# Optimization experiments

Hardware: AMD Instinct MI355X
Metric: run time of the kernel (lower is better)

The kernel has to match this reference:

```python
import jax, jax.numpy as jnp
import numpy as np

P1 = np.uint32(2654435761)
P2 = np.uint32(805459861)

LEVELS = 16
N_MIN = 16
GROWTH = 1.5
TABLE_SIZE = 524288
FEAT_DIM = 2


def _make_seeds_u32(levels):
    cA = np.uint64(15485907386658061715)
    cB = np.uint64(11400714819323198485)
    ls = np.arange(levels, dtype=np.uint64)
    u = (cA ^ (ls * cB))  # uint64 wraparound
    return (u & np.uint64(0xFFFFFFFF)).astype(np.uint32)


def setup_inputs() -> dict:
    key = jax.random.key(0)
    k1, k2, k3 = jax.random.split(key, 3)
    B = 8
    H = 256
    tile = 1024
    x0 = jax.random.uniform(k1, (B,), dtype=jnp.float32) * (tile - H)
    y0 = jax.random.uniform(k2, (B,), dtype=jnp.float32) * (tile - H)
    tables = jax.random.uniform(k3, (TABLE_SIZE, FEAT_DIM), dtype=jnp.float32,
                                minval=-0.01, maxval=0.01)
    seeds = jnp.asarray(_make_seeds_u32(LEVELS))
    level_N = jnp.asarray(
        [int(round(N_MIN * GROWTH ** l)) for l in range(LEVELS)], dtype=jnp.float32)
    return {"x0": x0, "y0": y0, "tables": tables, "seeds": seeds,
            "level_N": level_N, "memorized_crop_size": H,
            "complete_tile_size": tile}


def _hash2d(ix, iy, seed_u, T):
    # Instant-NGP style spatial hash, uint32 wraparound, per-level seed.
    h = (ix.astype(jnp.uint32) * P1) ^ (iy.astype(jnp.uint32) * P2) ^ seed_u
    return (h % jnp.uint32(T)).astype(jnp.int32)


def reference(x0, y0, tables, seeds, level_N, memorized_crop_size, complete_tile_size):
    B = x0.shape[0]
    H = W = int(memorized_crop_size)
    L = seeds.shape[0]
    T, F = tables.shape
    N = H * W

    xs = jnp.arange(H, dtype=jnp.float32)
    yy, xx = jnp.meshgrid(xs, xs, indexing='ij')          # [H, W]
    pxf = (xx[None] + x0[:, None, None]).reshape(B, N)     # [B, N]
    pyf = (yy[None] + y0[:, None, None]).reshape(B, N)

    scales = level_N / jnp.float32(complete_tile_size)     # [L]
    xyn_x = pxf[:, None, :] * scales[None, :, None]        # [B, L, N]
    xyn_y = pyf[:, None, :] * scales[None, :, None]

    ix0 = jnp.floor(xyn_x).astype(jnp.int32)
    iy0 = jnp.floor(xyn_y).astype(jnp.int32)
    ix1 = ix0 + 1
    iy1 = iy0 + 1
    fx = (xyn_x - ix0)[..., None]                          # [B, L, N, 1]
    fy = (xyn_y - iy0)[..., None]

    s = seeds[None, :, None]                               # [1, L, 1] uint32
    f00 = tables[_hash2d(ix0, iy0, s, T)]                  # [B, L, N, F]
    f10 = tables[_hash2d(ix1, iy0, s, T)]
    f01 = tables[_hash2d(ix0, iy1, s, T)]
    f11 = tables[_hash2d(ix1, iy1, s, T)]

    enc = ((1.0 - fx) * (1.0 - fy) * f00 + fx * (1.0 - fy) * f10
           + (1.0 - fx) * fy * f01 + fx * fy * f11)        # [B, L, N, F]

    enc = jnp.transpose(enc, (0, 2, 1, 3)).reshape(B, H, W, L * F)
    return jnp.transpose(enc, (0, 3, 1, 2))                # [B, L*F, H, W]
```

## Files before the change

kernel.cpp:

```cpp
#include <hip/hip_runtime.h>
#include <stdint.h>

#define HASH_T 524288u
#define HASH_MASK (HASH_T - 1u)
#define PRIME1 2654435761u
#define PRIME2 805459861u

__global__ __launch_bounds__(256) void lia_hashgrid_kernel(
    const float* __restrict__ x0,
    const float* __restrict__ y0,
    const float* __restrict__ tables,
    const uint32_t* __restrict__ seeds,
    const float* __restrict__ level_N,
    const int* __restrict__ tile_p,
    float* __restrict__ out)
{
    const int gid = blockIdx.x * 256 + threadIdx.x;
    const int j = gid & 255;
    const int i = (gid >> 8) & 255;
    const int bh = gid >> 16;
    const int half = bh & 1;
    const int b = bh >> 1;

    const float inv_tile = 1.0f / (float)(*tile_p);
    const float px = (float)j + x0[b];
    const float py = (float)i + y0[b];

    const float2* __restrict__ tab2 = (const float2*)tables;
    float* outp = out + ((size_t)b * 32u + (size_t)half * 16u) * 65536u
                      + (size_t)(i * 256 + j);

    const int lbase = half * 8;

    #pragma unroll
    for (int ll = 0; ll < 8; ++ll) {
        const int l = lbase + ll;
        const float scale = level_N[l] * inv_tile;
        const uint32_t seed = seeds[l];

        const float xn = px * scale;
        const float yn = py * scale;
        const float flx = floorf(xn);
        const float fly = floorf(yn);
        const float fx = xn - flx;
        const float fy = yn - fly;
        const uint32_t ix0 = (uint32_t)(int)flx;
        const uint32_t iy0 = (uint32_t)(int)fly;

        const uint32_t hx0 = ix0 * PRIME1;
        const uint32_t hx1 = hx0 + PRIME1;
        const uint32_t hy0 = iy0 * PRIME2;
        const uint32_t hy1 = hy0 + PRIME2;

        const uint32_t h00 = (hx0 ^ hy0 ^ seed) & HASH_MASK;
        const uint32_t h10 = (hx1 ^ hy0 ^ seed) & HASH_MASK;
        const uint32_t h01 = (hx0 ^ hy1 ^ seed) & HASH_MASK;
        const uint32_t h11 = (hx1 ^ hy1 ^ seed) & HASH_MASK;

        const float2 f00 = tab2[h00];
        const float2 f10 = tab2[h10];
        const float2 f01 = tab2[h01];
        const float2 f11 = tab2[h11];

        const float gx = 1.0f - fx;
        const float gy = 1.0f - fy;
        const float w00 = gx * gy;
        const float w10 = fx * gy;
        const float w01 = gx * fy;
        const float w11 = fx * fy;

        const float e0 = w00 * f00.x + w10 * f10.x + w01 * f01.x + w11 * f11.x;
        const float e1 = w00 * f00.y + w10 * f10.y + w01 * f01.y + w11 * f11.y;

        __builtin_nontemporal_store(e0, &outp[(size_t)(2 * ll) * 65536u]);
        __builtin_nontemporal_store(e1, &outp[(size_t)(2 * ll + 1) * 65536u]);
    }
}

extern "C" void kernel_launch(void* const* d_in, const int* in_sizes, int n_in,
                              void* d_out, int out_size, void* d_ws, size_t ws_size,
                              hipStream_t stream) {
    const float*    x0      = (const float*)d_in[0];
    const float*    y0      = (const float*)d_in[1];
    const float*    tables  = (const float*)d_in[2];
    const uint32_t* seeds   = (const uint32_t*)d_in[3];
    const float*    level_N = (const float*)d_in[4];
    const int*      tile_p  = (const int*)d_in[6];
    float*          out     = (float*)d_out;

    const int B = in_sizes[0];
    const int n_threads = B * 2 * 256 * 256;
    const int n_blocks = n_threads / 256;

    lia_hashgrid_kernel<<<n_blocks, 256, 0, stream>>>(
        x0, y0, tables, seeds, level_N, tile_p, out);
}
```

Before: 70.99 us.

## Process four pixels per thread, sharing corner gathers and vectorizing stores

Each thread now computes four adjacent pixels in x, so coarse levels can gather a small shared set of corner table entries and select among them instead of doing four gathers per pixel. Output stores become 16-byte vector nontemporal stores. Work is split unevenly across the two halves: one half handles levels 0-10 and the other levels 11-15, to balance gather counts. Correctness depends on the assumption that at most one (or four) cell boundaries are crossed within four pixels at those level scales. The grid also shrinks by four, which cuts thread count and occupancy.

```diff
diff --git a/kernel.cpp b/kernel.cpp
--- a/kernel.cpp
+++ b/kernel.cpp
@@ -5,6 +5,8 @@
 #define HASH_MASK (HASH_T - 1u)
 #define PRIME1 2654435761u
 #define PRIME2 805459861u
+
+typedef float f32x4 __attribute__((ext_vector_type(4)));
 
 __global__ __launch_bounds__(256) void lia_hashgrid_kernel(
     const float* __restrict__ x0,
@@ -16,64 +18,161 @@
     float* __restrict__ out)
 {
     const int gid = blockIdx.x * 256 + threadIdx.x;
-    const int j = gid & 255;
-    const int i = (gid >> 8) & 255;
-    const int bh = gid >> 16;
+    const int j0 = (gid & 63) << 2;
+    const int i  = (gid >> 6) & 255;
+    const int bh = gid >> 14;
     const int half = bh & 1;
     const int b = bh >> 1;
 
     const float inv_tile = 1.0f / (float)(*tile_p);
-    const float px = (float)j + x0[b];
+    const float xb = x0[b];
     const float py = (float)i + y0[b];
 
     const float2* __restrict__ tab2 = (const float2*)tables;
-    float* outp = out + ((size_t)b * 32u + (size_t)half * 16u) * 65536u
-                      + (size_t)(i * 256 + j);
+    float* outp = out + (size_t)b * 32u * 65536u + (size_t)(i * 256 + j0);
 
-    const int lbase = half * 8;
+    if (half == 0) {
+        #pragma unroll
+        for (int l = 0; l < 8; ++l) {
+            const float s = level_N[l] * inv_tile;
+            const uint32_t seed = seeds[l];
 
-    #pragma unroll
-    for (int ll = 0; ll < 8; ++ll) {
-        const int l = lbase + ll;
-        const float scale = level_N[l] * inv_tile;
-        const uint32_t seed = seeds[l];
+            const float yn = py * s;
+            const float fy = yn - floorf(yn);
+            const uint32_t iy0 = (uint32_t)(int)floorf(yn);
+            const uint32_t hy0 = iy0 * PRIME2;
+            const uint32_t hy1 = hy0 + PRIME2;
 
-        const float xn = px * scale;
-        const float yn = py * scale;
-        const float flx = floorf(xn);
-        const float fly = floorf(yn);
-        const float fx = xn - flx;
-        const float fy = yn - fly;
-        const uint32_t ix0 = (uint32_t)(int)flx;
-        const uint32_t iy0 = (uint32_t)(int)fly;
+            const float xn0 = ((float)j0 + xb) * s;
+            const float flx0 = floorf(xn0);
+            const uint32_t X = (uint32_t)(int)flx0;
+            const uint32_t hx0 = X * PRIME1;
+            const uint32_t hx1 = hx0 + PRIME1;
+            const uint32_t hx2 = hx1 + PRIME1;
 
-        const uint32_t hx0 = ix0 * PRIME1;
-        const uint32_t hx1 = hx0 + PRIME1;
-        const uint32_t hy0 = iy0 * PRIME2;
-        const uint32_t hy1 = hy0 + PRIME2;
+            const float2 t00 = tab2[(hx0 ^ hy0 ^ seed) & HASH_MASK];
+            const float2 t10 = tab2[(hx1 ^ hy0 ^ seed) & HASH_MASK];
+            const float2 t20 = tab2[(hx2 ^ hy0 ^ seed) & HASH_MASK];
+            const float2 t01 = tab2[(hx0 ^ hy1 ^ seed) & HASH_MASK];
+            const float2 t11 = tab2[(hx1 ^ hy1 ^ seed) & HASH_MASK];
+            const float2 t21 = tab2[(hx2 ^ hy1 ^ seed) & HASH_MASK];
 
-        const uint32_t h00 = (hx0 ^ hy0 ^ seed) & HASH_MASK;
-        const uint32_t h10 = (hx1 ^ hy0 ^ seed) & HASH_MASK;
-        const uint32_t h01 = (hx0 ^ hy1 ^ seed) & HASH_MASK;
-        const uint32_t h11 = (hx1 ^ hy1 ^ seed) & HASH_MASK;
+            const float gy = 1.0f - fy;
+            float e0s[4], e1s[4];
+            #pragma unroll
+            for (int p = 0; p < 4; ++p) {
+                const float xn = ((float)(j0 + p) + xb) * s;
+                const float flx = floorf(xn);
+                const float fx = xn - flx;
+                const bool dd = ((int)flx - (int)flx0) != 0;
+                const float2 f00 = dd ? t10 : t00;
+                const float2 f10 = dd ? t20 : t10;
+                const float2 f01 = dd ? t11 : t01;
+                const float2 f11 = dd ? t21 : t11;
+                const float gx = 1.0f - fx;
+                const float w00 = gx * gy, w10 = fx * gy;
+                const float w01 = gx * fy, w11 = fx * fy;
+                e0s[p] = w00 * f00.x + w10 * f10.x + w01 * f01.x + w11 * f11.x;
+                e1s[p] = w00 * f00.y + w10 * f10.y + w01 * f01.y + w11 * f11.y;
+            }
+            f32x4 v0 = {e0s[0], e0s[1], e0s[2], e0s[3]};
+            f32x4 v1 = {e1s[0], e1s[1], e1s[2], e1s[3]};
+            __builtin_nontemporal_store(v0, (f32x4*)(outp + (size_t)(2 * l) * 65536u));
+            __builtin_nontemporal_store(v1, (f32x4*)(outp + (size_t)(2 * l + 1) * 65536u));
+        }
+        #pragma unroll
+        for (int l = 8; l < 11; ++l) {
+            const float s = level_N[l] * inv_tile;
+            const uint32_t seed = seeds[l];
 
-        const float2 f00 = tab2[h00];
-        const float2 f10 = tab2[h10];
-        const float2 f01 = tab2[h01];
-        const float2 f11 = tab2[h11];
+            const float yn = py * s;
+            const float fy = yn - floorf(yn);
+            const uint32_t iy0 = (uint32_t)(int)floorf(yn);
+            const uint32_t hy0 = iy0 * PRIME2;
+            const uint32_t hy1 = hy0 + PRIME2;
 
-        const float gx = 1.0f - fx;
-        const float gy = 1.0f - fy;
-        const float w00 = gx * gy;
-        const float w10 = fx * gy;
-        const float w01 = gx * fy;
-        const float w11 = fx * fy;
+            const float xn0 = ((float)j0 + xb) * s;
+            const float flx0 = floorf(xn0);
+            const uint32_t X = (uint32_t)(int)flx0;
+            const uint32_t hx0 = X * PRIME1;
+            const uint32_t hx1 = hx0 + PRIME1;
+            const uint32_t hx2 = hx1 + PRIME1;
+            const uint32_t hx3 = hx2 + PRIME1;
+            const uint32_t hx4 = hx3 + PRIME1;
 
-        const float e0 = w00 * f00.x + w10 * f10.x + w01 * f01.x + w11 * f11.x;
-        const float e1 = w00 * f00.y + w10 * f10.y + w01 * f01.y + w11 * f11.y;
+            const float2 t0a = tab2[(hx0 ^ hy0 ^ seed) & HASH_MASK];
+            const float2 t1a = tab2[(hx1 ^ hy0 ^ seed) & HASH_MASK];
+            const float2 t2a = tab2[(hx2 ^ hy0 ^ seed) & HASH_MASK];
+            const float2 t3a = tab2[(hx3 ^ hy0 ^ seed) & HASH_MASK];
+            const float2 t4a = tab2[(hx4 ^ hy0 ^ seed) & HASH_MASK];
+            const float2 t0b = tab2[(hx0 ^ hy1 ^ seed) & HASH_MASK];
+            const float2 t1b = tab2[(hx1 ^ hy1 ^ seed) & HASH_MASK];
+            const float2 t2b = tab2[(hx2 ^ hy1 ^ seed) & HASH_MASK];
+            const float2 t3b = tab2[(hx3 ^ hy1 ^ seed) & HASH_MASK];
+            const float2 t4b = tab2[(hx4 ^ hy1 ^ seed) & HASH_MASK];
 
-        __builtin_nontemporal_store(e0, &outp[(size_t)(2 * ll) * 65536u]);
-        __builtin_nontemporal_store(e1, &outp[(size_t)(2 * ll + 1) * 65536u]);
+            const float gy = 1.0f - fy;
+            float e0s[4], e1s[4];
+            #pragma unroll
+            for (int p = 0; p < 4; ++p) {
+                const float xn = ((float)(j0 + p) + xb) * s;
+                const float flx = floorf(xn);
+                const float fx = xn - flx;
+                const int d = (int)flx - (int)flx0;
+                const float2 f00 = d == 0 ? t0a : d == 1 ? t1a : d == 2 ? t2a : t3a;
+                const float2 f10 = d == 0 ? t1a : d == 1 ? t2a : d == 2 ? t3a : t4a;
+                const float2 f01 = d == 0 ? t0b : d == 1 ? t1b : d == 2 ? t2b : t3b;
+                const float2 f11 = d == 0 ? t1b : d == 1 ? t2b : d == 2 ? t3b : t4b;
+                const float gx = 1.0f - fx;
+                const float w00 = gx * gy, w10 = fx * gy;
+                const float w01 = gx * fy, w11 = fx * fy;
+                e0s[p] = w00 * f00.x + w10 * f10.x + w01 * f01.x + w11 * f11.x;
+                e1s[p] = w00 * f00.y + w10 * f10.y + w01 * f01.y + w11 * f11.y;
+            }
+            f32x4 v0 = {e0s[0], e0s[1], e0s[2], e0s[3]};
+            f32x4 v1 = {e1s[0], e1s[1], e1s[2], e1s[3]};
+            __builtin_nontemporal_store(v0, (f32x4*)(outp + (size_t)(2 * l) * 65536u));
+            __builtin_nontemporal_store(v1, (f32x4*)(outp + (size_t)(2 * l + 1) * 65536u));
+        }
+    } else {
+        #pragma unroll
+        for (int l = 11; l < 16; ++l) {
+            const float s = level_N[l] * inv_tile;
+            const uint32_t seed = seeds[l];
+
+            const float yn = py * s;
+            const float fy = yn - floorf(yn);
+            const uint32_t iy0 = (uint32_t)(int)floorf(yn);
+            const uint32_t hy0 = iy0 * PRIME2;
+            const uint32_t hy1 = hy0 + PRIME2;
+            const float gy = 1.0f - fy;
+
+            float e0s[4], e1s[4];
+            #pragma unroll
+            for (int p = 0; p < 4; ++p) {
+                const float xn = ((float)(j0 + p) + xb) * s;
+                const float flx = floorf(xn);
+                const float fx = xn - flx;
+                const uint32_t ix0 = (uint32_t)(int)flx;
+                const uint32_t hx0 = ix0 * PRIME1;
+                const uint32_t hx1 = hx0 + PRIME1;
+
+                const float2 f00 = tab2[(hx0 ^ hy0 ^ seed) & HASH_MASK];
+                const float2 f10 = tab2[(hx1 ^ hy0 ^ seed) & HASH_MASK];
+                const float2 f01 = tab2[(hx0 ^ hy1 ^ seed) & HASH_MASK];
+                const float2 f11 = tab2[(hx1 ^ hy1 ^ seed) & HASH_MASK];
+
+                const float gx = 1.0f - fx;
+                const float w00 = gx * gy, w10 = fx * gy;
+                const float w01 = gx * fy, w11 = fx * fy;
+                e0s[p] = w00 * f00.x + w10 * f10.x + w01 * f01.x + w11 * f11.x;
+                e1s[p] = w00 * f00.y + w10 * f10.y + w01 * f01.y + w11 * f11.y;
+            }
+            f32x4 v0 = {e0s[0], e0s[1], e0s[2], e0s[3]};
+            f32x4 v1 = {e1s[0], e1s[1], e1s[2], e1s[3]};
+            __builtin_nontemporal_store(v0, (f32x4*)(outp + (size_t)(2 * l) * 65536u));
+            __builtin_nontemporal_store(v1, (f32x4*)(outp + (size_t)(2 * l + 1) * 65536u));
+        }
     }
 }
 
@@ -89,7 +188,7 @@
     float*          out     = (float*)d_out;
 
     const int B = in_sizes[0];
-    const int n_threads = B * 2 * 256 * 256;
+    const int n_threads = B * 2 * 256 * 64;
     const int n_blocks = n_threads / 256;
 
     lia_hashgrid_kernel<<<n_blocks, 256, 0, stream>>>(
```

Result: slower. 87.11 us (+22.7%).

## Process two adjacent pixels per thread, sharing corner lookups on coarse levels

Applied to the files above, without the earlier changes.

Each thread now computes two horizontally adjacent pixels. On the coarse levels (0-10) it fetches a 3x2 set of table corners and reuses them for both pixels, selecting the right corners depending on whether the pixels fall in different cells. This cuts gather count, and the output is written with 8-byte vector nontemporal stores. The level split between block halves is changed to 11/5 to roughly balance the work. Each thread does more work and there are half as many blocks, so latency hiding for the random gathers on fine levels may suffer.

```diff
diff --git a/kernel.cpp b/kernel.cpp
--- a/kernel.cpp
+++ b/kernel.cpp
@@ -5,6 +5,8 @@
 #define HASH_MASK (HASH_T - 1u)
 #define PRIME1 2654435761u
 #define PRIME2 805459861u
+
+typedef float f32x2 __attribute__((ext_vector_type(2)));
 
 __global__ __launch_bounds__(256) void lia_hashgrid_kernel(
     const float* __restrict__ x0,
@@ -15,65 +17,114 @@
     const int* __restrict__ tile_p,
     float* __restrict__ out)
 {
-    const int gid = blockIdx.x * 256 + threadIdx.x;
-    const int j = gid & 255;
-    const int i = (gid >> 8) & 255;
-    const int bh = gid >> 16;
-    const int half = bh & 1;
-    const int b = bh >> 1;
+    const int bid  = blockIdx.x;
+    const int half = bid & 1;
+    const int rest = bid >> 1;
+    const int b    = rest >> 7;
+    const int tid  = threadIdx.x;
+    const int i    = (((rest & 127) << 1) | (tid >> 7));
+    const int j0   = (tid & 127) << 1;
 
     const float inv_tile = 1.0f / (float)(*tile_p);
-    const float px = (float)j + x0[b];
+    const float xb = x0[b];
     const float py = (float)i + y0[b];
 
     const float2* __restrict__ tab2 = (const float2*)tables;
-    float* outp = out + ((size_t)b * 32u + (size_t)half * 16u) * 65536u
-                      + (size_t)(i * 256 + j);
+    float* outp = out + (size_t)b * 32u * 65536u + (size_t)(i * 256 + j0);
 
-    const int lbase = half * 8;
+    if (half == 0) {
+        #pragma unroll
+        for (int l = 0; l < 11; ++l) {
+            const float s = level_N[l] * inv_tile;
+            const uint32_t seed = seeds[l];
 
-    #pragma unroll
-    for (int ll = 0; ll < 8; ++ll) {
-        const int l = lbase + ll;
-        const float scale = level_N[l] * inv_tile;
-        const uint32_t seed = seeds[l];
+            const float yn = py * s;
+            const float fy = yn - floorf(yn);
+            const uint32_t iy0 = (uint32_t)(int)floorf(yn);
+            const uint32_t hy0 = iy0 * PRIME2;
+            const uint32_t hy1 = hy0 + PRIME2;
+            const float gy = 1.0f - fy;
 
-        const float xn = px * scale;
-        const float yn = py * scale;
-        const float flx = floorf(xn);
-        const float fly = floorf(yn);
-        const float fx = xn - flx;
-        const float fy = yn - fly;
-        const uint32_t ix0 = (uint32_t)(int)flx;
-        const uint32_t iy0 = (uint32_t)(int)fly;
+            const float xnA = ((float)j0 + xb) * s;
+            const float xnB = ((float)(j0 + 1) + xb) * s;
+            const float flxA = floorf(xnA);
+            const float flxB = floorf(xnB);
+            const float fxA = xnA - flxA;
+            const float fxB = xnB - flxB;
+            const uint32_t X = (uint32_t)(int)flxA;
+            const bool dB = ((int)flxB - (int)flxA) != 0;
 
-        const uint32_t hx0 = ix0 * PRIME1;
-        const uint32_t hx1 = hx0 + PRIME1;
-        const uint32_t hy0 = iy0 * PRIME2;
-        const uint32_t hy1 = hy0 + PRIME2;
+            const uint32_t hx0 = X * PRIME1;
+            const uint32_t hx1 = hx0 + PRIME1;
+            const uint32_t hx2 = hx1 + PRIME1;
 
-        const uint32_t h00 = (hx0 ^ hy0 ^ seed) & HASH_MASK;
-        const uint32_t h10 = (hx1 ^ hy0 ^ seed) & HASH_MASK;
-        const uint32_t h01 = (hx0 ^ hy1 ^ seed) & HASH_MASK;
-        const uint32_t h11 = (hx1 ^ hy1 ^ seed) & HASH_MASK;
+            const float2 t0a = tab2[(hx0 ^ hy0 ^ seed) & HASH_MASK];
+            const float2 t1a = tab2[(hx1 ^ hy0 ^ seed) & HASH_MASK];
+            const float2 t2a = tab2[(hx2 ^ hy0 ^ seed) & HASH_MASK];
+            const float2 t0b = tab2[(hx0 ^ hy1 ^ seed) & HASH_MASK];
+            const float2 t1b = tab2[(hx1 ^ hy1 ^ seed) & HASH_MASK];
+            const float2 t2b = tab2[(hx2 ^ hy1 ^ seed) & HASH_MASK];
 
-        const float2 f00 = tab2[h00];
-        const float2 f10 = tab2[h10];
-        const float2 f01 = tab2[h01];
-        const float2 f11 = tab2[h11];
+            const float gxA = 1.0f - fxA;
+            const float w00A = gxA * gy, w10A = fxA * gy;
+            const float w01A = gxA * fy, w11A = fxA * fy;
+            const float e0A = w00A * t0a.x + w10A * t1a.x + w01A * t0b.x + w11A * t1b.x;
+            const float e1A = w00A * t0a.y + w10A * t1a.y + w01A * t0b.y + w11A * t1b.y;
 
-        const float gx = 1.0f - fx;
-        const float gy = 1.0f - fy;
-        const float w00 = gx * gy;
-        const float w10 = fx * gy;
-        const float w01 = gx * fy;
-        const float w11 = fx * fy;
+            const float2 f00 = dB ? t1a : t0a;
+            const float2 f10 = dB ? t2a : t1a;
+            const float2 f01 = dB ? t1b : t0b;
+            const float2 f11 = dB ? t2b : t1b;
+            const float gxB = 1.0f - fxB;
+            const float w00B = gxB * gy, w10B = fxB * gy;
+            const float w01B = gxB * fy, w11B = fxB * fy;
+            const float e0B = w00B * f00.x + w10B * f10.x + w01B * f01.x + w11B * f11.x;
+            const float e1B = w00B * f00.y + w10B * f10.y + w01B * f01.y + w11B * f11.y;
 
-        const float e0 = w00 * f00.x + w10 * f10.x + w01 * f01.x + w11 * f11.x;
-        const float e1 = w00 * f00.y + w10 * f10.y + w01 * f01.y + w11 * f11.y;
+            f32x2 v0 = {e0A, e0B};
+            f32x2 v1 = {e1A, e1B};
+            __builtin_nontemporal_store(v0, (f32x2*)(outp + (size_t)(2 * l) * 65536u));
+            __builtin_nontemporal_store(v1, (f32x2*)(outp + (size_t)(2 * l + 1) * 65536u));
+        }
+    } else {
+        #pragma unroll
+        for (int l = 11; l < 16; ++l) {
+            const float s = level_N[l] * inv_tile;
+            const uint32_t seed = seeds[l];
 
-        __builtin_nontemporal_store(e0, &outp[(size_t)(2 * ll) * 65536u]);
-        __builtin_nontemporal_store(e1, &outp[(size_t)(2 * ll + 1) * 65536u]);
+            const float yn = py * s;
+            const float fy = yn - floorf(yn);
+            const uint32_t iy0 = (uint32_t)(int)floorf(yn);
+            const uint32_t hy0 = iy0 * PRIME2;
+            const uint32_t hy1 = hy0 + PRIME2;
+            const float gy = 1.0f - fy;
+
+            float e0s[2], e1s[2];
+            #pragma unroll
+            for (int p = 0; p < 2; ++p) {
+                const float xn = ((float)(j0 + p) + xb) * s;
+                const float flx = floorf(xn);
+                const float fx = xn - flx;
+                const uint32_t ix0 = (uint32_t)(int)flx;
+                const uint32_t hx0 = ix0 * PRIME1;
+                const uint32_t hx1 = hx0 + PRIME1;
+
+                const float2 f00 = tab2[(hx0 ^ hy0 ^ seed) & HASH_MASK];
+                const float2 f10 = tab2[(hx1 ^ hy0 ^ seed) & HASH_MASK];
+                const float2 f01 = tab2[(hx0 ^ hy1 ^ seed) & HASH_MASK];
+                const float2 f11 = tab2[(hx1 ^ hy1 ^ seed) & HASH_MASK];
+
+                const float gx = 1.0f - fx;
+                const float w00 = gx * gy, w10 = fx * gy;
+                const float w01 = gx * fy, w11 = fx * fy;
+                e0s[p] = w00 * f00.x + w10 * f10.x + w01 * f01.x + w11 * f11.x;
+                e1s[p] = w00 * f00.y + w10 * f10.y + w01 * f01.y + w11 * f11.y;
+            }
+            f32x2 v0 = {e0s[0], e0s[1]};
+            f32x2 v1 = {e1s[0], e1s[1]};
+            __builtin_nontemporal_store(v0, (f32x2*)(outp + (size_t)(2 * l) * 65536u));
+            __builtin_nontemporal_store(v1, (f32x2*)(outp + (size_t)(2 * l + 1) * 65536u));
+        }
     }
 }
 
@@ -89,8 +140,7 @@
     float*          out     = (float*)d_out;
 
     const int B = in_sizes[0];
-    const int n_threads = B * 2 * 256 * 256;
-    const int n_blocks = n_threads / 256;
+    const int n_blocks = B * 128 * 2;
 
     lia_hashgrid_kernel<<<n_blocks, 256, 0, stream>>>(
         x0, y0, tables, seeds, level_N, tile_p, out);
```

New measurement: 91.21 us. 28.5% more time.
